# Optimization experiments

Measured on AMD Instinct MI355X. Metric: run time of the kernel, lower is better.

The kernel has to match this reference:

```python
import jax, jax.numpy as jnp
import numpy as np

N = 204800   # total nodes (4096 subgraphs x 50 nodes)
E = 3276800  # edges (avg degree 16)
B = 4096     # number of subgraphs
IN = 64      # in_feats
HID = 32     # latent_dim per layer
CAT = 128    # 4 * 32 concatenated states
PH = 64      # pooling hidden dim
R = 3        # num_relations
NB = 2       # num_bases
MARGIN = 1.0


def setup_inputs() -> dict:
    key = jax.random.key(0)
    ks = jax.random.split(key, 24)
    s = 0.1
    inp = {}
    inp['x'] = jax.random.normal(ks[0], (N, IN), jnp.float32)
    inp['edge_norm'] = jax.random.uniform(ks[1], (E,), jnp.float32)
    inp['src'] = jax.random.randint(ks[2], (E,), 0, N, jnp.int32)
    inp['dst'] = jax.random.randint(ks[3], (E,), 0, N, jnp.int32)
    inp['etype'] = jax.random.randint(ks[4], (E,), 0, R, jnp.int32)
    inp['graph_id'] = jnp.arange(N, dtype=jnp.int32) // (N // B)
    inp['ntype'] = jax.random.randint(ks[5], (N,), 0, 2, jnp.int32)
    # layer 0: basis-decomposed RelGraphConv (in=64 -> 32)
    inp['bases0'] = jax.random.normal(ks[6], (NB, IN, HID), jnp.float32) * s
    inp['coef0'] = jax.random.normal(ks[7], (R, NB), jnp.float32)
    inp['wself0'] = jax.random.normal(ks[8], (IN, HID), jnp.float32) * s
    inp['bias0'] = jnp.zeros((HID,), jnp.float32)
    # layers 1..3 stacked (32 -> 32 each)
    inp['bases_r'] = jax.random.normal(ks[9], (3, NB, HID, HID), jnp.float32) * s
    inp['coef_r'] = jax.random.normal(ks[10], (3, R, NB), jnp.float32)
    inp['wself_r'] = jax.random.normal(ks[11], (3, HID, HID), jnp.float32) * s
    inp['bias_r'] = jnp.zeros((3, HID), jnp.float32)
    # attention pooling (user / item)
    inp['wp_u'] = jax.random.normal(ks[12], (CAT, PH), jnp.float32) * s
    inp['wt_u'] = jax.random.normal(ks[13], (CAT, PH), jnp.float32) * s
    inp['wp_i'] = jax.random.normal(ks[14], (CAT, PH), jnp.float32) * s
    inp['wt_i'] = jax.random.normal(ks[15], (CAT, PH), jnp.float32) * s
    # MLP head
    inp['w1'] = jax.random.normal(ks[16], (2 * PH, 64), jnp.float32) * s
    inp['b1'] = jnp.zeros((64,), jnp.float32)
    inp['w2'] = jax.random.normal(ks[17], (64, 1), jnp.float32) * s
    inp['b2'] = jnp.zeros((1,), jnp.float32)
    return inp


def _rgcn_layer(h, bases, coef, wself, bias, src, dst, etype, edge_norm):
    # basis decomposition: W_r = sum_b coef[r,b] * bases[b]
    W = jnp.einsum('rb,bio->rio', coef, bases)          # [R, in, out]
    xr = jnp.einsum('ni,rio->nro', h, W)                # [N, R, out] (transform then gather)
    msg = xr[src, etype] * edge_norm[:, None]           # [E, out]
    agg = jax.ops.segment_sum(msg, dst, num_segments=N) # scatter-add to dst
    return jnp.tanh(agg + h @ wself + bias)


def _attn_pool(x, mask, gid, wp, wt):
    # x: [N, CAT], mask: [N] bool (target node type), gid: [N] graph ids
    fmask = mask.astype(x.dtype)
    cnt = jax.ops.segment_sum(fmask, gid, num_segments=B)              # [B]
    tmean = jax.ops.segment_sum(x * fmask[:, None], gid, num_segments=B)
    tmean = tmean / (cnt[:, None] + 1e-8)                              # [B, CAT]
    p = x @ wp                                                          # [N, PH]
    t = tmean @ wt                                                      # [B, PH]
    score = jnp.sum(p * t[gid], axis=-1) / jnp.sqrt(jnp.float32(PH))    # [N]
    score = jnp.where(mask, score, -1e9)
    m = jax.ops.segment_max(score, gid, num_segments=B)                 # [B]
    a = jnp.exp(score - m[gid]) * fmask
    z = jax.ops.segment_sum(a, gid, num_segments=B)
    alpha = a / (z[gid] + 1e-8)
    return jax.ops.segment_sum(alpha[:, None] * p, gid, num_segments=B)  # [B, PH]


def reference(x, edge_norm, src, dst, etype, graph_id, ntype,
              bases0, coef0, wself0, bias0, bases_r, coef_r, wself_r, bias_r,
              wp_u, wt_u, wp_i, wt_i, w1, b1, w2, b2):
    h = x
    states = []
    h = _rgcn_layer(h, bases0, coef0, wself0, bias0, src, dst, etype, edge_norm)
    states.append(h)
    for l in range(3):
        h = _rgcn_layer(h, bases_r[l], coef_r[l], wself_r[l], bias_r[l],
                        src, dst, etype, edge_norm)
        states.append(h)
    hcat = jnp.concatenate(states, axis=1)  # [N, 128]

    mask_u = ntype == 0
    mask_i = ntype == 1

    # triplet contrastive loss over per-graph mean user/item embeddings
    fu = mask_u.astype(hcat.dtype)
    fi = mask_i.astype(hcat.dtype)
    cu = jax.ops.segment_sum(fu, graph_id, num_segments=B) + 1e-8
    ci = jax.ops.segment_sum(fi, graph_id, num_segments=B) + 1e-8
    au = jax.ops.segment_sum(hcat * fu[:, None], graph_id, num_segments=B) / cu[:, None]
    ai = jax.ops.segment_sum(hcat * fi[:, None], graph_id, num_segments=B) / ci[:, None]
    an = jnp.roll(ai, 1, axis=0)  # negatives from shifted graphs
    dpos = jnp.sum((au - ai) ** 2, axis=-1)
    dneg = jnp.sum((au - an) ** 2, axis=-1)
    triplet_loss = jnp.mean(jax.nn.relu(dpos - dneg + MARGIN))

    x_u = _attn_pool(hcat, mask_u, graph_id, wp_u, wt_u)  # [B, 64]
    x_i = _attn_pool(hcat, mask_i, graph_id, wp_i, wt_i)  # [B, 64]
    z = jnp.concatenate([x_u, x_i], axis=1)               # [B, 128]
    z = jax.nn.relu(z @ w1 + b1)                          # dropout off (eval)
    out = jax.nn.sigmoid(z @ w2 + b2)[:, 0]               # [B]
    return out, triplet_loss
```

## Files before the change

### kernel.cpp

```cpp
#include <hip/hip_runtime.h>
#include <cstdint>
#include <cstddef>

#define NN   204800
#define EE   3276800
#define BB   4096
#define GS   50
#define NBUCK 200
#define CHUNK 8192
#define BCAP  17408

typedef __attribute__((ext_vector_type(8))) short short8v;
typedef __attribute__((ext_vector_type(4))) float f32x4;

__device__ __forceinline__ float bf2f(unsigned short u) {
  unsigned int x = ((unsigned int)u) << 16;
  return __int_as_float((int)x);
}
__device__ __forceinline__ unsigned short f2bf(float f) {
  unsigned int x = __float_as_uint(f);
  unsigned int r = (x + 0x7fffu + ((x >> 16) & 1u)) >> 16;
  return (unsigned short)r;
}

__global__ __launch_bounds__(256) void init_cursor_kernel(int* __restrict__ gcursor) {
  const int t = threadIdx.x;
  if (t < NBUCK) gcursor[t] = t * BCAP;
}

__global__ __launch_bounds__(256) void pass1_kernel(const int* __restrict__ src,
                                                    const int* __restrict__ dst,
                                                    const int* __restrict__ etype,
                                                    const float* __restrict__ en,
                                                    int* __restrict__ gcursor,
                                                    int2* __restrict__ staging) {
  __shared__ int2 stage[CHUNK];
  __shared__ unsigned char bid[CHUNK];
  __shared__ int hist[NBUCK], cur[NBUCK], lo[NBUCK], gbase[NBUCK];
  __shared__ int sc[256];
  const int tid = threadIdx.x;
  const int ebase = blockIdx.x * CHUNK;

  for (int i = tid; i < NBUCK; i += 256) hist[i] = 0;
  __syncthreads();
  for (int i = tid; i < CHUNK; i += 256) {
    int bk = dst[ebase + i] >> 10;
    bid[i] = (unsigned char)bk;
    atomicAdd(&hist[bk], 1);
  }
  __syncthreads();
  int hv = (tid < NBUCK) ? hist[tid] : 0;
  sc[tid] = hv;
  __syncthreads();
  for (int off = 1; off < 256; off <<= 1) {
    int t = (tid >= off) ? sc[tid - off] : 0;
    __syncthreads();
    sc[tid] += t;
    __syncthreads();
  }
  if (tid < NBUCK) {
    int excl = sc[tid] - hv;
    lo[tid]  = excl;
    cur[tid] = excl;
    gbase[tid] = hv ? atomicAdd(&gcursor[tid], hv) : 0;
  }
  __syncthreads();
  for (int i = tid; i < CHUNK; i += 256) {
    int bk = bid[i];
    int p = atomicAdd(&cur[bk], 1);
    int s  = src[ebase + i];
    int et = etype[ebase + i];
    int d  = dst[ebase + i];
    int2 r;
    r.x = (s << 12) | (et << 10) | (d & 1023);
    r.y = __float_as_int(en[ebase + i]);
    stage[p] = r;
  }
  __syncthreads();
  const int wave = tid >> 6, lane = tid & 63;
  for (int bk = wave; bk < NBUCK; bk += 4) {
    const int len = hist[bk];
    const int l0  = lo[bk];
    const int gb  = gbase[bk];
    for (int i = lane; i < len; i += 64)
      staging[gb + i] = stage[l0 + i];
  }
}

__global__ __launch_bounds__(256) void pass2_kernel(const int2* __restrict__ staging,
                                                    const int* __restrict__ gcursor,
                                                    int* __restrict__ begs,
                                                    int* __restrict__ ends,
                                                    int2* __restrict__ edata) {
  __shared__ int lhist[1024];
  __shared__ int lcur[1024];
  __shared__ int psum[256];
  const int b = blockIdx.x;
  const int tid = threadIdx.x;
  const int base = b * BCAP;
  const int cnt  = gcursor[b] - base;

  for (int i = tid; i < 1024; i += 256) lhist[i] = 0;
  __syncthreads();
  for (int i = tid; i < cnt; i += 256)
    atomicAdd(&lhist[staging[base + i].x & 1023], 1);
  __syncthreads();
  int s0 = lhist[4 * tid], s1 = lhist[4 * tid + 1];
  int s2 = lhist[4 * tid + 2], s3 = lhist[4 * tid + 3];
  int tot = s0 + s1 + s2 + s3;
  psum[tid] = tot;
  __syncthreads();
  for (int off = 1; off < 256; off <<= 1) {
    int t = (tid >= off) ? psum[tid - off] : 0;
    __syncthreads();
    psum[tid] += t;
    __syncthreads();
  }
  int o0 = base + psum[tid] - tot;
  int o1 = o0 + s0, o2 = o1 + s1, o3 = o2 + s2;
  const int nodeb = b * 1024;
  begs[nodeb + 4 * tid]     = o0;  ends[nodeb + 4 * tid]     = o1;  lcur[4 * tid]     = o0;
  begs[nodeb + 4 * tid + 1] = o1;  ends[nodeb + 4 * tid + 1] = o2;  lcur[4 * tid + 1] = o1;
  begs[nodeb + 4 * tid + 2] = o2;  ends[nodeb + 4 * tid + 2] = o3;  lcur[4 * tid + 2] = o2;
  begs[nodeb + 4 * tid + 3] = o3;  ends[nodeb + 4 * tid + 3] = o3 + s3;  lcur[4 * tid + 3] = o3;
  __syncthreads();
  for (int i = tid; i < cnt; i += 256) {
    int2 r = staging[base + i];
    int pos = atomicAdd(&lcur[r.x & 1023], 1);
    int s  = r.x >> 12;
    int et = (r.x >> 10) & 3;
    int2 outr;
    outr.x = (s << 8) + (et << 6);
    outr.y = r.y;
    edata[pos] = outr;
  }
}

__global__ __launch_bounds__(256) void wprep_kernel(
    const float* __restrict__ bases0, const float* __restrict__ coef0,
    const float* __restrict__ wself0,
    const float* __restrict__ bases_r, const float* __restrict__ coef_r,
    const float* __restrict__ wself_r,
    const float* __restrict__ wp_u, const float* __restrict__ wp_i,
    const float* __restrict__ wt_u, const float* __restrict__ wt_i,
    const float* __restrict__ w1,
    float* __restrict__ Wbuf) {
  int idx = blockIdx.x * 256 + threadIdx.x;
  if (idx < 8192) {
    int i = idx >> 7, j = idx & 127;
    float v;
    if (j < 96) {
      int r = j >> 5, f = j & 31;
      v = coef0[r * 2 + 0] * bases0[0 * 2048 + i * 32 + f]
        + coef0[r * 2 + 1] * bases0[1 * 2048 + i * 32 + f];
    } else {
      v = wself0[i * 32 + (j - 96)];
    }
    Wbuf[idx] = v;
    return;
  }
  int idx2 = idx - 8192;
  if (idx2 < 3 * 4096) {
    int l = idx2 >> 12, rem = idx2 & 4095;
    int i = rem >> 7, j = rem & 127;
    float v;
    if (j < 96) {
      int r = j >> 5, f = j & 31;
      v = coef_r[l * 6 + r * 2 + 0] * bases_r[l * 2048 + 0 * 1024 + i * 32 + f]
        + coef_r[l * 6 + r * 2 + 1] * bases_r[l * 2048 + 1 * 1024 + i * 32 + f];
    } else {
      v = wself_r[l * 1024 + i * 32 + (j - 96)];
    }
    Wbuf[idx] = v;
    return;
  }
  int idx3 = idx2 - 12288;
  if (idx3 < 32768) {
    int side = idx3 >> 14;
    int r = idx3 & 16383;
    int kk = r >> 7, k = r & 127;
    const float* wp = side ? wp_i : wp_u;
    const float* wt = side ? wt_i : wt_u;
    float acc = 0.f;
#pragma unroll 8
    for (int j = 0; j < 64; ++j)
      acc = fmaf(wp[k * 64 + j], wt[kk * 64 + j], acc);
    Wbuf[idx] = acc * 0.125f;
    return;
  }
  int idx4 = idx3 - 32768;
  if (idx4 < 16384) {
    int kp = idx4 >> 6, t = idx4 & 63;
    int side = kp >> 7, k = kp & 127;
    const float* wp = side ? wp_i : wp_u;
    float acc = 0.f;
#pragma unroll 8
    for (int j = 0; j < 64; ++j)
      acc = fmaf(wp[k * 64 + j], w1[(side * 64 + j) * 64 + t], acc);
    Wbuf[idx] = acc;
  }
}

__global__ __launch_bounds__(256) void wprep2_kernel(const float* __restrict__ Wbuf,
                                                     unsigned short* __restrict__ Whi,
                                                     unsigned short* __restrict__ Wlo) {
  int e = blockIdx.x * 256 + threadIdx.x;
  if (e >= 20480) return;
  float v;
  if (e < 8192) {
    int j = e & 7, l = (e >> 3) & 63, c = (e >> 9) & 7, q = e >> 12;
    int k   = q * 32 + (l >> 4) * 8 + j;
    int col = c * 16 + (l & 15);
    v = Wbuf[k * 128 + col];
  } else {
    int e2 = e - 8192;
    int lay = e2 >> 12, r = e2 & 4095;
    int j = r & 7, l = (r >> 3) & 63, qc = r >> 9;
    int q = qc >> 1, c = qc & 1;
    int k = q * 32 + (l >> 4) * 8 + j;
    int o = c * 16 + (l & 15);
    const float* Wc = Wbuf + 8192 + lay * 4096;
    v = (k < 96) ? Wc[(k & 31) * 128 + (k >> 5) * 32 + o]
                 : Wc[(k - 96) * 128 + 96 + o];
  }
  unsigned short hi = f2bf(v);
  Whi[e] = hi;
  Wlo[e] = f2bf(v - bf2f(hi));
}

__global__ __launch_bounds__(256) void cvt_bf16_kernel(const float* __restrict__ in,
                                                       unsigned short* __restrict__ hi,
                                                       unsigned short* __restrict__ lo,
                                                       int n4) {
  int i = blockIdx.x * 256 + threadIdx.x;
  if (i < n4) {
    const float4 a = reinterpret_cast<const float4*>(in)[i];
    ushort4 h, l;
    h.x = f2bf(a.x); l.x = f2bf(a.x - bf2f(h.x));
    h.y = f2bf(a.y); l.y = f2bf(a.y - bf2f(h.y));
    h.z = f2bf(a.z); l.z = f2bf(a.z - bf2f(h.z));
    h.w = f2bf(a.w); l.w = f2bf(a.w - bf2f(h.w));
    reinterpret_cast<ushort4*>(hi)[i] = h;
    reinterpret_cast<ushort4*>(lo)[i] = l;
  }
}

__global__ __launch_bounds__(256) void transform_l0_kernel(
    const unsigned short* __restrict__ Ahi, const unsigned short* __restrict__ Alo,
    const unsigned short* __restrict__ Whi, const unsigned short* __restrict__ Wlo,
    unsigned short* __restrict__ Tb0) {
  __shared__ float C[64][129];
  const int tid = threadIdx.x;
  const int wv = tid >> 6, l = tid & 63;
  const int l15 = l & 15, kg = l >> 4;
  const int row = blockIdx.x * 64 + wv * 16 + l15;

  short8v ah[2], al[2];
#pragma unroll
  for (int q = 0; q < 2; ++q) {
    ah[q] = *reinterpret_cast<const short8v*>(Ahi + (size_t)row * 64 + q * 32 + kg * 8);
    al[q] = *reinterpret_cast<const short8v*>(Alo + (size_t)row * 64 + q * 32 + kg * 8);
  }

#pragma unroll
  for (int c = 0; c < 8; ++c) {
    f32x4 a = {0.f, 0.f, 0.f, 0.f};
#pragma unroll
    for (int q = 0; q < 2; ++q) {
      const size_t fb = ((size_t)(q * 8 + c) * 64 + l) * 8;
      const short8v bh = *reinterpret_cast<const short8v*>(Whi + fb);
      const short8v bl = *reinterpret_cast<const short8v*>(Wlo + fb);
      a = __builtin_amdgcn_mfma_f32_16x16x32_bf16(ah[q], bh, a, 0, 0, 0);
      a = __builtin_amdgcn_mfma_f32_16x16x32_bf16(al[q], bh, a, 0, 0, 0);
      a = __builtin_amdgcn_mfma_f32_16x16x32_bf16(ah[q], bl, a, 0, 0, 0);
    }
#pragma unroll
    for (int r = 0; r < 4; ++r)
      C[wv * 16 + kg * 4 + r][c * 16 + l15] = a[r];
  }
  __syncthreads();

  const int row64 = tid & 63, q = tid >> 6;
  const int node = blockIdx.x * 64 + row64;
#pragma unroll
  for (int v = 0; v < 4; ++v) {
    const int cb = q * 32 + v * 8;
    uint4 pk;
    pk.x = (unsigned)f2bf(C[row64][cb + 0]) | ((unsigned)f2bf(C[row64][cb + 1]) << 16);
    pk.y = (unsigned)f2bf(C[row64][cb + 2]) | ((unsigned)f2bf(C[row64][cb + 3]) << 16);
    pk.z = (unsigned)f2bf(C[row64][cb + 4]) | ((unsigned)f2bf(C[row64][cb + 5]) << 16);
    pk.w = (unsigned)f2bf(C[row64][cb + 6]) | ((unsigned)f2bf(C[row64][cb + 7]) << 16);
    *reinterpret_cast<uint4*>(Tb0 + (size_t)node * 128 + cb) = pk;
  }
}

__global__ __launch_bounds__(256) void aggregate_l0_kernel(
    const unsigned short* __restrict__ Tb0,
    const int* __restrict__ begs, const int* __restrict__ ends,
    const int2* __restrict__ edata, const float* __restrict__ bias,
    float* __restrict__ hcat, unsigned short* __restrict__ Ab) {
  const int node = blockIdx.x * 32 + (threadIdx.x >> 3);
  const int f4   = (threadIdx.x & 7) * 4;
  const int loff = f4 * 2;
  const char* Tbc = (const char*)Tb0;
  const int beg = begs[node];
  const int end = ends[node];
  const ushort4 sb = *reinterpret_cast<const ushort4*>(Tbc + (size_t)node * 256 + 192 + loff);
  const float4 bv  = *reinterpret_cast<const float4*>(&bias[f4]);
  float ax = bf2f(sb.x) + bv.x, ay = bf2f(sb.y) + bv.y;
  float az = bf2f(sb.z) + bv.z, aw = bf2f(sb.w) + bv.w;

  int k = beg;
  for (; k + 8 <= end; k += 8) {
    int2 ed[8];
#pragma unroll
    for (int u = 0; u < 8; ++u) ed[u] = edata[k + u];
    ushort4 mv[8];
#pragma unroll
    for (int u = 0; u < 8; ++u)
      mv[u] = *reinterpret_cast<const ushort4*>(Tbc + ed[u].x + loff);
#pragma unroll
    for (int u = 0; u < 8; ++u) {
      const float nm = __int_as_float(ed[u].y);
      ax = fmaf(bf2f(mv[u].x), nm, ax);
      ay = fmaf(bf2f(mv[u].y), nm, ay);
      az = fmaf(bf2f(mv[u].z), nm, az);
      aw = fmaf(bf2f(mv[u].w), nm, aw);
    }
  }
  for (; k < end; ++k) {
    int2 e0 = edata[k];
    const float nm = __int_as_float(e0.y);
    ushort4 m0 = *reinterpret_cast<const ushort4*>(Tbc + e0.x + loff);
    ax = fmaf(bf2f(m0.x), nm, ax);
    ay = fmaf(bf2f(m0.y), nm, ay);
    az = fmaf(bf2f(m0.z), nm, az);
    aw = fmaf(bf2f(m0.w), nm, aw);
  }
  float4 o;
  o.x = tanhf(ax); o.y = tanhf(ay); o.z = tanhf(az); o.w = tanhf(aw);
  *reinterpret_cast<float4*>(&hcat[(size_t)node * 128 + f4]) = o;
  ushort4 h;
  h.x = f2bf(o.x); h.y = f2bf(o.y); h.z = f2bf(o.z); h.w = f2bf(o.w);
  *reinterpret_cast<ushort4*>(Ab + (size_t)node * 128 + 96 + f4) = h;
}

__global__ __launch_bounds__(256) void aggregate_raw_kernel(
    unsigned short* __restrict__ Ab,
    const int* __restrict__ begs, const int* __restrict__ ends,
    const int2* __restrict__ edata) {
  const int node = blockIdx.x * 32 + (threadIdx.x >> 3);
  const int f4   = (threadIdx.x & 7) * 4;
  const int loff = f4 * 2;
  const char* Abc = (const char*)Ab;
  const int beg = begs[node];
  const int end = ends[node];
  float a0x = 0.f, a0y = 0.f, a0z = 0.f, a0w = 0.f;
  float a1x = 0.f, a1y = 0.f, a1z = 0.f, a1w = 0.f;
  float a2x = 0.f, a2y = 0.f, a2z = 0.f, a2w = 0.f;

  int k = beg;
  for (; k + 8 <= end; k += 8) {
    int2 ed[8];
#pragma unroll
    for (int u = 0; u < 8; ++u) ed[u] = edata[k + u];
    ushort4 mv[8];
#pragma unroll
    for (int u = 0; u < 8; ++u)
      mv[u] = *reinterpret_cast<const ushort4*>(Abc + (ed[u].x & ~255) + 192 + loff);
#pragma unroll
    for (int u = 0; u < 8; ++u) {
      const int et = (ed[u].x >> 6) & 3;
      const float nm = __int_as_float(ed[u].y);
      const float n0 = (et == 0) ? nm : 0.f;
      const float n1 = (et == 1) ? nm : 0.f;
      const float n2 = (et == 2) ? nm : 0.f;
      const float vx = bf2f(mv[u].x), vy = bf2f(mv[u].y);
      const float vz = bf2f(mv[u].z), vw = bf2f(mv[u].w);
      a0x = fmaf(vx, n0, a0x); a0y = fmaf(vy, n0, a0y);
      a0z = fmaf(vz, n0, a0z); a0w = fmaf(vw, n0, a0w);
      a1x = fmaf(vx, n1, a1x); a1y = fmaf(vy, n1, a1y);
      a1z = fmaf(vz, n1, a1z); a1w = fmaf(vw, n1, a1w);
      a2x = fmaf(vx, n2, a2x); a2y = fmaf(vy, n2, a2y);
      a2z = fmaf(vz, n2, a2z); a2w = fmaf(vw, n2, a2w);
    }
  }
  for (; k < end; ++k) {
    int2 e0 = edata[k];
    const int et = (e0.x >> 6) & 3;
    const float nm = __int_as_float(e0.y);
    const float n0 = (et == 0) ? nm : 0.f;
    const float n1 = (et == 1) ? nm : 0.f;
    const float n2 = (et == 2) ? nm : 0.f;
    ushort4 m0 = *reinterpret_cast<const ushort4*>(Abc + (e0.x & ~255) + 192 + loff);
    const float vx = bf2f(m0.x), vy = bf2f(m0.y), vz = bf2f(m0.z), vw = bf2f(m0.w);
    a0x = fmaf(vx, n0, a0x); a0y = fmaf(vy, n0, a0y);
    a0z = fmaf(vz, n0, a0z); a0w = fmaf(vw, n0, a0w);
    a1x = fmaf(vx, n1, a1x); a1y = fmaf(vy, n1, a1y);
    a1z = fmaf(vz, n1, a1z); a1w = fmaf(vw, n1, a1w);
    a2x = fmaf(vx, n2, a2x); a2y = fmaf(vy, n2, a2y);
    a2z = fmaf(vz, n2, a2z); a2w = fmaf(vw, n2, a2w);
  }
  ushort4 s0, s1, s2;
  s0.x = f2bf(a0x); s0.y = f2bf(a0y); s0.z = f2bf(a0z); s0.w = f2bf(a0w);
  s1.x = f2bf(a1x); s1.y = f2bf(a1y); s1.z = f2bf(a1z); s1.w = f2bf(a1w);
  s2.x = f2bf(a2x); s2.y = f2bf(a2y); s2.z = f2bf(a2z); s2.w = f2bf(a2w);
  unsigned short* rowp = Ab + (size_t)node * 128;
  *reinterpret_cast<ushort4*>(rowp + f4)      = s0;
  *reinterpret_cast<ushort4*>(rowp + 32 + f4) = s1;
  *reinterpret_cast<ushort4*>(rowp + 64 + f4) = s2;
}

__global__ __launch_bounds__(256) void transform_new_kernel(
    const unsigned short* __restrict__ Ab,
    const unsigned short* __restrict__ Whi, const unsigned short* __restrict__ Wlo,
    const float* __restrict__ bias,
    float* __restrict__ hcatSlot, unsigned short* __restrict__ AbY) {
  __shared__ float C[64][33];
  const int tid = threadIdx.x;
  const int wv = tid >> 6, l = tid & 63;
  const int l15 = l & 15, kg = l >> 4;
  const int row = blockIdx.x * 64 + wv * 16 + l15;

  short8v af[4];
#pragma unroll
  for (int q = 0; q < 4; ++q)
    af[q] = *reinterpret_cast<const short8v*>(Ab + (size_t)row * 128 + q * 32 + kg * 8);

#pragma unroll
  for (int c = 0; c < 2; ++c) {
    f32x4 a = {0.f, 0.f, 0.f, 0.f};
#pragma unroll
    for (int q = 0; q < 4; ++q) {
      const size_t fb = ((size_t)(q * 2 + c) * 64 + l) * 8;
      const short8v bh = *reinterpret_cast<const short8v*>(Whi + fb);
      const short8v bl = *reinterpret_cast<const short8v*>(Wlo + fb);
      a = __builtin_amdgcn_mfma_f32_16x16x32_bf16(af[q], bh, a, 0, 0, 0);
      a = __builtin_amdgcn_mfma_f32_16x16x32_bf16(af[q], bl, a, 0, 0, 0);
    }
#pragma unroll
    for (int r = 0; r < 4; ++r)
      C[wv * 16 + kg * 4 + r][c * 16 + l15] = a[r];
  }
  __syncthreads();

  const int row64 = tid & 63, g = tid >> 6;
  const int node = blockIdx.x * 64 + row64;
  float z[8];
#pragma unroll
  for (int v = 0; v < 8; ++v)
    z[v] = tanhf(C[row64][g * 8 + v] + bias[g * 8 + v]);
  float4 f0 = {z[0], z[1], z[2], z[3]};
  float4 f1 = {z[4], z[5], z[6], z[7]};
  *reinterpret_cast<float4*>(hcatSlot + (size_t)node * 128 + g * 8)     = f0;
  *reinterpret_cast<float4*>(hcatSlot + (size_t)node * 128 + g * 8 + 4) = f1;
  if (AbY) {
    uint4 pk;
    pk.x = (unsigned)f2bf(z[0]) | ((unsigned)f2bf(z[1]) << 16);
    pk.y = (unsigned)f2bf(z[2]) | ((unsigned)f2bf(z[3]) << 16);
    pk.z = (unsigned)f2bf(z[4]) | ((unsigned)f2bf(z[5]) << 16);
    pk.w = (unsigned)f2bf(z[6]) | ((unsigned)f2bf(z[7]) << 16);
    *reinterpret_cast<uint4*>(AbY + (size_t)node * 128 + 96 + g * 8) = pk;
  }
}

__global__ __launch_bounds__(256) void pool_head_kernel(
    const float* __restrict__ hcat, const int* __restrict__ ntype,
    const float* __restrict__ Mt,
    const float* __restrict__ W1c,
    const float* __restrict__ b1,
    const float* __restrict__ w2, const float* __restrict__ b2,
    float* __restrict__ out, float* __restrict__ tl) {
  __shared__ float hl[GS * 129];
  __shared__ float scr[1024];
  __shared__ float av2[256];
  __shared__ float red[4];
  __shared__ float cnts[4];
  __shared__ int   snt[64];
  __shared__ int   sntp[64];

  const int g    = (blockIdx.x & 7) * (BB / 8) + (blockIdx.x >> 3);
  const int gp   = (g + BB - 1) & (BB - 1);
  const int tid  = threadIdx.x;
  const int lane = tid & 63;

  const float* hg  = hcat + (size_t)g  * (GS * 128);
  const float* hp  = hcat + (size_t)gp * (GS * 128);
  const int*   ntg = ntype + g  * GS;
  const int*   ntp = ntype + gp * GS;

  if (tid < 64) {
    snt[tid] = (tid < GS) ? ntg[tid] : 99;
    unsigned long long bu = __ballot(snt[tid] == 0);
    unsigned long long bi = __ballot(snt[tid] == 1);
    if (lane == 0) {
      cnts[0] = 1.f / ((float)__popcll(bu) + 1e-8f);
      cnts[1] = 1.f / ((float)__popcll(bi) + 1e-8f);
    }
  } else if (tid < 128) {
    sntp[lane] = (lane < GS) ? ntp[lane] : 99;
    unsigned long long bp = __ballot(sntp[lane] == 1);
    if (lane == 0) cnts[2] = 1.f / ((float)__popcll(bp) + 1e-8f);
  }

  {
    const int rowg = tid >> 5;
    const int kq   = (tid & 31) * 4;
    float spx = 0.f, spy = 0.f, spz = 0.f, spw = 0.f;
#pragma unroll
    for (int p = 0; p < 7; ++p) {
      const int r = rowg + 8 * p;
      if (r < GS) {
        const float4 v = *reinterpret_cast<const float4*>(hg + r * 128 + kq);
        hl[r * 129 + kq + 0] = v.x;
        hl[r * 129 + kq + 1] = v.y;
        hl[r * 129 + kq + 2] = v.z;
        hl[r * 129 + kq + 3] = v.w;
        if (ntp[r] == 1) {
          const float4 w = *reinterpret_cast<const float4*>(hp + r * 128 + kq);
          spx += w.x; spy += w.y; spz += w.z; spw += w.w;
        }
      }
    }
    scr[rowg * 128 + kq + 0] = spx;
    scr[rowg * 128 + kq + 1] = spy;
    scr[rowg * 128 + kq + 2] = spz;
    scr[rowg * 128 + kq + 3] = spw;
  }
  __syncthreads();

  if (tid < 128) {
    const int kf = tid;
    float su = 0.f, si = 0.f;
#pragma unroll
    for (int r = 0; r < GS; ++r) {
      const float v = hl[r * 129 + kf];
      if (snt[r] == 0) su += v; else si += v;
    }
    float sp = 0.f;
#pragma unroll
    for (int rg = 0; rg < 8; ++rg) sp += scr[rg * 128 + kf];
    const float auk = su * cnts[0];
    const float aik = si * cnts[1];
    const float apk = sp * cnts[2];
    av2[kf]       = auk;
    av2[128 + kf] = aik;
    float d1 = (auk - aik) * (auk - aik);
    float d2 = (auk - apk) * (auk - apk);
    for (int o = 32; o; o >>= 1) {
      d1 += __shfl_xor(d1, o);
      d2 += __shfl_xor(d2, o);
    }
    if (lane == 0) { red[tid >> 6] = d1; red[2 + (tid >> 6)] = d2; }
  }
  __syncthreads();

  {
    const int side = tid >> 7, kf = tid & 127;
    const float* M  = Mt + (size_t)side * 16384 + kf;
    const float* av = av2 + side * 128;
    float a0 = 0.f, a1 = 0.f, a2 = 0.f, a3 = 0.f;
#pragma unroll 4
    for (int kk = 0; kk < 128; kk += 4) {
      a0 = fmaf(M[(kk + 0) * 128], av[kk + 0], a0);
      a1 = fmaf(M[(kk + 1) * 128], av[kk + 1], a1);
      a2 = fmaf(M[(kk + 2) * 128], av[kk + 2], a2);
      a3 = fmaf(M[(kk + 3) * 128], av[kk + 3], a3);
    }
    scr[tid] = (a0 + a1) + (a2 + a3);
  }
  if (tid == 0) tl[g] = fmaxf(0.f, (red[0] + red[1]) - (red[2] + red[3]) + 1.0f);
  __syncthreads();

  if (tid < 128) {
    const int side = tid >> 6;
    const float* q = scr + side * 128;
    float v = -1e9f;
    bool msk = false;
    if (lane < GS) {
      msk = (snt[lane] == side);
      float a0 = 0.f, a1 = 0.f;
#pragma unroll 8
      for (int k = 0; k < 128; k += 2) {
        a0 = fmaf(hl[lane * 129 + k], q[k], a0);
        a1 = fmaf(hl[lane * 129 + k + 1], q[k + 1], a1);
      }
      v = msk ? (a0 + a1) : -1e9f;
    }
    float m = v;
    for (int o = 32; o; o >>= 1) m = fmaxf(m, __shfl_xor(m, o));
    float e = (lane < GS && msk) ? expf(v - m) : 0.f;
    float z = e;
    for (int o = 32; o; o >>= 1) z += __shfl_xor(z, o);
    const float invz = 1.f / (z + 1e-8f);
    if (lane < GS) scr[256 + side * 64 + lane] = e * invz;
  }
  __syncthreads();

  {
    const int side = tid >> 7, kf = tid & 127;
    const float* a = scr + 256 + side * 64;
    float acc = 0.f;
#pragma unroll
    for (int nl = 0; nl < GS; ++nl)
      acc = fmaf(a[nl], hl[nl * 129 + kf], acc);
    scr[384 + side * 128 + kf] = acc;
  }
  __syncthreads();

  {
    const int j = tid & 63, c = tid >> 6;
    const float* Wc = W1c + (size_t)c * 64 * 64 + j;
    const float* cv = scr + 384 + c * 64;
    float a0 = 0.f, a1 = 0.f, a2 = 0.f, a3 = 0.f;
#pragma unroll 4
    for (int k = 0; k < 64; k += 4) {
      a0 = fmaf(Wc[(k + 0) * 64], cv[k + 0], a0);
      a1 = fmaf(Wc[(k + 1) * 64], cv[k + 1], a1);
      a2 = fmaf(Wc[(k + 2) * 64], cv[k + 2], a2);
      a3 = fmaf(Wc[(k + 3) * 64], cv[k + 3], a3);
    }
    scr[640 + c * 64 + j] = (a0 + a1) + (a2 + a3);
  }
  __syncthreads();

  if (tid < 64) {
    const float z1 = fmaxf(b1[tid] + scr[640 + tid] + scr[704 + tid] +
                           scr[768 + tid] + scr[832 + tid], 0.f);
    float p = z1 * w2[tid];
    for (int o = 32; o; o >>= 1) p += __shfl_xor(p, o);
    if (tid == 0) out[g] = 1.f / (1.f + expf(-(p + b2[0])));
  }
}

__global__ __launch_bounds__(256) void tl_reduce_kernel(const float* __restrict__ tl,
                                                        float* __restrict__ out) {
  __shared__ float s[256];
  float acc = 0.f;
  for (int i = threadIdx.x; i < BB; i += 256) acc += tl[i];
  s[threadIdx.x] = acc;
  __syncthreads();
  for (int off = 128; off > 0; off >>= 1) {
    if (threadIdx.x < off) s[threadIdx.x] += s[threadIdx.x + off];
    __syncthreads();
  }
  if (threadIdx.x == 0) out[BB] = s[0] * (1.f / (float)BB);
}

extern "C" void kernel_launch(void* const* d_in, const int* in_sizes, int n_in,
                              void* d_out, int out_size, void* d_ws, size_t ws_size,
                              hipStream_t stream) {
  const float* x        = (const float*)d_in[0];
  const float* edge_nrm = (const float*)d_in[1];
  const int*   src      = (const int*)d_in[2];
  const int*   dst      = (const int*)d_in[3];
  const int*   etype    = (const int*)d_in[4];
  const int*   ntype    = (const int*)d_in[6];
  const float* bases0   = (const float*)d_in[7];
  const float* coef0    = (const float*)d_in[8];
  const float* wself0   = (const float*)d_in[9];
  const float* bias0    = (const float*)d_in[10];
  const float* bases_r  = (const float*)d_in[11];
  const float* coef_r   = (const float*)d_in[12];
  const float* wself_r  = (const float*)d_in[13];
  const float* bias_r   = (const float*)d_in[14];
  const float* wp_u     = (const float*)d_in[15];
  const float* wt_u     = (const float*)d_in[16];
  const float* wp_i     = (const float*)d_in[17];
  const float* wt_i     = (const float*)d_in[18];
  const float* w1       = (const float*)d_in[19];
  const float* b1       = (const float*)d_in[20];
  const float* w2       = (const float*)d_in[21];
  const float* b2       = (const float*)d_in[22];
  float* out = (float*)d_out;

  float*          hcat = (float*)d_ws;
  float*          R    = hcat + (size_t)NN * 128;
  int2*           staging = (int2*)R;
  unsigned short* Tb0  = (unsigned short*)R;
  unsigned short* AbA  = Tb0 + (size_t)NN * 128;
  unsigned short* AbB  = Tb0;
  unsigned short* A0hi = (unsigned short*)(hcat + (size_t)NN * 64);
  unsigned short* A0lo = A0hi + (size_t)NN * 64;
  int2*  edata   = (int2*)(R + (size_t)NN * 128);
  int*   begs    = (int*)(edata + (size_t)NBUCK * BCAP);
  int*   ends    = begs + NN;
  int*   gcursor = ends + NN;
  float* Wbuf    = (float*)(gcursor + 256);
  unsigned short* Whi = (unsigned short*)(Wbuf + 69632);
  unsigned short* Wlo = Whi + 20480;
  float* tl      = Wbuf + 69632 + 10240;

  size_t need = ((size_t)NN * 128 * 2 + (size_t)NBUCK * BCAP * 2 + 2 * NN + 256 +
                 69632 + 10240 + BB) * 4;
  if (ws_size < need) return;

  init_cursor_kernel<<<1, 256, 0, stream>>>(gcursor);
  pass1_kernel<<<EE / CHUNK, 256, 0, stream>>>(src, dst, etype, edge_nrm,
                                               gcursor, staging);
  pass2_kernel<<<NBUCK, 256, 0, stream>>>(staging, gcursor, begs, ends, edata);

  wprep_kernel<<<(69632 + 255) / 256, 256, 0, stream>>>(
      bases0, coef0, wself0, bases_r, coef_r, wself_r,
      wp_u, wp_i, wt_u, wt_i, w1, Wbuf);
  wprep2_kernel<<<80, 256, 0, stream>>>(Wbuf, Whi, Wlo);
  cvt_bf16_kernel<<<(NN * 64 / 4 + 255) / 256, 256, 0, stream>>>(
      x, A0hi, A0lo, NN * 64 / 4);

  transform_l0_kernel<<<NN / 64, 256, 0, stream>>>(A0hi, A0lo, Whi, Wlo, Tb0);
  aggregate_l0_kernel<<<NN / 32, 256, 0, stream>>>(Tb0, begs, ends, edata,
                                                   bias0, hcat, AbA);

  unsigned short* AbX[3] = {AbA, AbB, AbA};
  unsigned short* AbY[3] = {AbB, AbA, nullptr};
  for (int l = 1; l <= 3; ++l) {
    aggregate_raw_kernel<<<NN / 32, 256, 0, stream>>>(AbX[l - 1], begs, ends, edata);
    transform_new_kernel<<<NN / 64, 256, 0, stream>>>(
        AbX[l - 1], Whi + 8192 + (size_t)(l - 1) * 4096,
        Wlo + 8192 + (size_t)(l - 1) * 4096, bias_r + (l - 1) * 32,
        hcat + (size_t)l * 32, AbY[l - 1]);
  }

  pool_head_kernel<<<BB, 256, 0, stream>>>(hcat, ntype,
                                           Wbuf + 20480, Wbuf + 53248,
                                           b1, w2, b2, out, tl);
  tl_reduce_kernel<<<1, 256, 0, stream>>>(tl, out);
}
```

Before: 589.2 us.

## Fuse edge aggregation with per-layer transform and fold bf16 split into L0 transform

```diff
diff --git a/kernel.cpp b/kernel.cpp
--- a/kernel.cpp
+++ b/kernel.cpp
@@ -21,11 +21,6 @@
   unsigned int x = __float_as_uint(f);
   unsigned int r = (x + 0x7fffu + ((x >> 16) & 1u)) >> 16;
   return (unsigned short)r;
-}
-
-__global__ __launch_bounds__(256) void init_cursor_kernel(int* __restrict__ gcursor) {
-  const int t = threadIdx.x;
-  if (t < NBUCK) gcursor[t] = t * BCAP;
 }
 
 __global__ __launch_bounds__(256) void pass1_kernel(const int* __restrict__ src,
@@ -144,7 +139,9 @@
     const float* __restrict__ wp_u, const float* __restrict__ wp_i,
     const float* __restrict__ wt_u, const float* __restrict__ wt_i,
     const float* __restrict__ w1,
-    float* __restrict__ Wbuf) {
+    float* __restrict__ Wbuf, int* __restrict__ gcursor) {
+  if (blockIdx.x == 0 && threadIdx.x < NBUCK)
+    gcursor[threadIdx.x] = threadIdx.x * BCAP;
   int idx = blockIdx.x * 256 + threadIdx.x;
   if (idx < 8192) {
     int i = idx >> 7, j = idx & 127;
@@ -228,25 +225,8 @@
   Wlo[e] = f2bf(v - bf2f(hi));
 }
 
-__global__ __launch_bounds__(256) void cvt_bf16_kernel(const float* __restrict__ in,
-                                                       unsigned short* __restrict__ hi,
-                                                       unsigned short* __restrict__ lo,
-                                                       int n4) {
-  int i = blockIdx.x * 256 + threadIdx.x;
-  if (i < n4) {
-    const float4 a = reinterpret_cast<const float4*>(in)[i];
-    ushort4 h, l;
-    h.x = f2bf(a.x); l.x = f2bf(a.x - bf2f(h.x));
-    h.y = f2bf(a.y); l.y = f2bf(a.y - bf2f(h.y));
-    h.z = f2bf(a.z); l.z = f2bf(a.z - bf2f(h.z));
-    h.w = f2bf(a.w); l.w = f2bf(a.w - bf2f(h.w));
-    reinterpret_cast<ushort4*>(hi)[i] = h;
-    reinterpret_cast<ushort4*>(lo)[i] = l;
-  }
-}
-
 __global__ __launch_bounds__(256) void transform_l0_kernel(
-    const unsigned short* __restrict__ Ahi, const unsigned short* __restrict__ Alo,
+    const float* __restrict__ x,
     const unsigned short* __restrict__ Whi, const unsigned short* __restrict__ Wlo,
     unsigned short* __restrict__ Tb0) {
   __shared__ float C[64][129];
@@ -258,8 +238,16 @@
   short8v ah[2], al[2];
 #pragma unroll
   for (int q = 0; q < 2; ++q) {
-    ah[q] = *reinterpret_cast<const short8v*>(Ahi + (size_t)row * 64 + q * 32 + kg * 8);
-    al[q] = *reinterpret_cast<const short8v*>(Alo + (size_t)row * 64 + q * 32 + kg * 8);
+    const float* xp = x + (size_t)row * 64 + q * 32 + kg * 8;
+    const float4 v0 = *reinterpret_cast<const float4*>(xp);
+    const float4 v1 = *reinterpret_cast<const float4*>(xp + 4);
+    const float vv[8] = {v0.x, v0.y, v0.z, v0.w, v1.x, v1.y, v1.z, v1.w};
+#pragma unroll
+    for (int f = 0; f < 8; ++f) {
+      const unsigned short h = f2bf(vv[f]);
+      ah[q][f] = (short)h;
+      al[q][f] = (short)f2bf(vv[f] - bf2f(h));
+    }
   }
 
 #pragma unroll
@@ -298,7 +286,7 @@
     const unsigned short* __restrict__ Tb0,
     const int* __restrict__ begs, const int* __restrict__ ends,
     const int2* __restrict__ edata, const float* __restrict__ bias,
-    float* __restrict__ hcat, unsigned short* __restrict__ Ab) {
+    float* __restrict__ hcat, unsigned short* __restrict__ hbA) {
   const int node = blockIdx.x * 32 + (threadIdx.x >> 3);
   const int f4   = (threadIdx.x & 7) * 4;
   const int loff = f4 * 2;
@@ -342,125 +330,128 @@
   *reinterpret_cast<float4*>(&hcat[(size_t)node * 128 + f4]) = o;
   ushort4 h;
   h.x = f2bf(o.x); h.y = f2bf(o.y); h.z = f2bf(o.z); h.w = f2bf(o.w);
-  *reinterpret_cast<ushort4*>(Ab + (size_t)node * 128 + 96 + f4) = h;
-}
-
-__global__ __launch_bounds__(256) void aggregate_raw_kernel(
-    unsigned short* __restrict__ Ab,
+  *reinterpret_cast<ushort4*>(hbA + (size_t)node * 32 + f4) = h;
+}
+
+__global__ __launch_bounds__(256) void agg_tf_kernel(
+    const unsigned short* __restrict__ hbX,
     const int* __restrict__ begs, const int* __restrict__ ends,
-    const int2* __restrict__ edata) {
-  const int node = blockIdx.x * 32 + (threadIdx.x >> 3);
-  const int f4   = (threadIdx.x & 7) * 4;
-  const int loff = f4 * 2;
-  const char* Abc = (const char*)Ab;
-  const int beg = begs[node];
-  const int end = ends[node];
-  float a0x = 0.f, a0y = 0.f, a0z = 0.f, a0w = 0.f;
-  float a1x = 0.f, a1y = 0.f, a1z = 0.f, a1w = 0.f;
-  float a2x = 0.f, a2y = 0.f, a2z = 0.f, a2w = 0.f;
-
-  int k = beg;
-  for (; k + 8 <= end; k += 8) {
-    int2 ed[8];
-#pragma unroll
-    for (int u = 0; u < 8; ++u) ed[u] = edata[k + u];
-    ushort4 mv[8];
-#pragma unroll
-    for (int u = 0; u < 8; ++u)
-      mv[u] = *reinterpret_cast<const ushort4*>(Abc + (ed[u].x & ~255) + 192 + loff);
-#pragma unroll
-    for (int u = 0; u < 8; ++u) {
-      const int et = (ed[u].x >> 6) & 3;
-      const float nm = __int_as_float(ed[u].y);
+    const int2* __restrict__ edata,
+    const unsigned short* __restrict__ Whi, const unsigned short* __restrict__ Wlo,
+    const float* __restrict__ bias,
+    float* __restrict__ hcatSlot, unsigned short* __restrict__ hbY) {
+  __shared__ __align__(16) unsigned short sld[64][136];
+  __shared__ float C[64][33];
+  const int tid = threadIdx.x;
+
+  {
+    const int nl   = tid >> 2;
+    const int node = blockIdx.x * 64 + nl;
+    const int f8   = (tid & 3) * 8;
+    const int loff = f8 * 2;
+    const char* hbc = (const char*)hbX;
+    const int beg = begs[node], end = ends[node];
+    float a0[8], a1[8], a2[8];
+#pragma unroll
+    for (int f = 0; f < 8; ++f) { a0[f] = 0.f; a1[f] = 0.f; a2[f] = 0.f; }
+
+    int k = beg;
+    for (; k + 8 <= end; k += 8) {
+      int2 ed[8];
+#pragma unroll
+      for (int u = 0; u < 8; ++u) ed[u] = edata[k + u];
+      short8v mv[8];
+#pragma unroll
+      for (int u = 0; u < 8; ++u)
+        mv[u] = *reinterpret_cast<const short8v*>(hbc + ((ed[u].x >> 2) & ~63) + loff);
+#pragma unroll
+      for (int u = 0; u < 8; ++u) {
+        const int et = (ed[u].x >> 6) & 3;
+        const float nm = __int_as_float(ed[u].y);
+        const float n0 = (et == 0) ? nm : 0.f;
+        const float n1 = (et == 1) ? nm : 0.f;
+        const float n2 = (et == 2) ? nm : 0.f;
+#pragma unroll
+        for (int f = 0; f < 8; ++f) {
+          const float v = bf2f((unsigned short)mv[u][f]);
+          a0[f] = fmaf(v, n0, a0[f]);
+          a1[f] = fmaf(v, n1, a1[f]);
+          a2[f] = fmaf(v, n2, a2[f]);
+        }
+      }
+    }
+    for (; k < end; ++k) {
+      int2 e0 = edata[k];
+      const int et = (e0.x >> 6) & 3;
+      const float nm = __int_as_float(e0.y);
       const float n0 = (et == 0) ? nm : 0.f;
       const float n1 = (et == 1) ? nm : 0.f;
       const float n2 = (et == 2) ? nm : 0.f;
-      const float vx = bf2f(mv[u].x), vy = bf2f(mv[u].y);
-      const float vz = bf2f(mv[u].z), vw = bf2f(mv[u].w);
-      a0x = fmaf(vx, n0, a0x); a0y = fmaf(vy, n0, a0y);
-      a0z = fmaf(vz, n0, a0z); a0w = fmaf(vw, n0, a0w);
-      a1x = fmaf(vx, n1, a1x); a1y = fmaf(vy, n1, a1y);
-      a1z = fmaf(vz, n1, a1z); a1w = fmaf(vw, n1, a1w);
-      a2x = fmaf(vx, n2, a2x); a2y = fmaf(vy, n2, a2y);
-      a2z = fmaf(vz, n2, a2z); a2w = fmaf(vw, n2, a2w);
-    }
-  }
-  for (; k < end; ++k) {
-    int2 e0 = edata[k];
-    const int et = (e0.x >> 6) & 3;
-    const float nm = __int_as_float(e0.y);
-    const float n0 = (et == 0) ? nm : 0.f;
-    const float n1 = (et == 1) ? nm : 0.f;
-    const float n2 = (et == 2) ? nm : 0.f;
-    ushort4 m0 = *reinterpret_cast<const ushort4*>(Abc + (e0.x & ~255) + 192 + loff);
-    const float vx = bf2f(m0.x), vy = bf2f(m0.y), vz = bf2f(m0.z), vw = bf2f(m0.w);
-    a0x = fmaf(vx, n0, a0x); a0y = fmaf(vy, n0, a0y);
-    a0z = fmaf(vz, n0, a0z); a0w = fmaf(vw, n0, a0w);
-    a1x = fmaf(vx, n1, a1x); a1y = fmaf(vy, n1, a1y);
-    a1z = fmaf(vz, n1, a1z); a1w = fmaf(vw, n1, a1w);
-    a2x = fmaf(vx, n2, a2x); a2y = fmaf(vy, n2, a2y);
-    a2z = fmaf(vz, n2, a2z); a2w = fmaf(vw, n2, a2w);
-  }
-  ushort4 s0, s1, s2;
-  s0.x = f2bf(a0x); s0.y = f2bf(a0y); s0.z = f2bf(a0z); s0.w = f2bf(a0w);
-  s1.x = f2bf(a1x); s1.y = f2bf(a1y); s1.z = f2bf(a1z); s1.w = f2bf(a1w);
-  s2.x = f2bf(a2x); s2.y = f2bf(a2y); s2.z = f2bf(a2z); s2.w = f2bf(a2w);
-  unsigned short* rowp = Ab + (size_t)node * 128;
-  *reinterpret_cast<ushort4*>(rowp + f4)      = s0;
-  *reinterpret_cast<ushort4*>(rowp + 32 + f4) = s1;
-  *reinterpret_cast<ushort4*>(rowp + 64 + f4) = s2;
-}
-
-__global__ __launch_bounds__(256) void transform_new_kernel(
-    const unsigned short* __restrict__ Ab,
-    const unsigned short* __restrict__ Whi, const unsigned short* __restrict__ Wlo,
-    const float* __restrict__ bias,
-    float* __restrict__ hcatSlot, unsigned short* __restrict__ AbY) {
-  __shared__ float C[64][33];
-  const int tid = threadIdx.x;
-  const int wv = tid >> 6, l = tid & 63;
-  const int l15 = l & 15, kg = l >> 4;
-  const int row = blockIdx.x * 64 + wv * 16 + l15;
-
-  short8v af[4];
-#pragma unroll
-  for (int q = 0; q < 4; ++q)
-    af[q] = *reinterpret_cast<const short8v*>(Ab + (size_t)row * 128 + q * 32 + kg * 8);
-
-#pragma unroll
-  for (int c = 0; c < 2; ++c) {
-    f32x4 a = {0.f, 0.f, 0.f, 0.f};
-#pragma unroll
-    for (int q = 0; q < 4; ++q) {
-      const size_t fb = ((size_t)(q * 2 + c) * 64 + l) * 8;
-      const short8v bh = *reinterpret_cast<const short8v*>(Whi + fb);
-      const short8v bl = *reinterpret_cast<const short8v*>(Wlo + fb);
-      a = __builtin_amdgcn_mfma_f32_16x16x32_bf16(af[q], bh, a, 0, 0, 0);
-      a = __builtin_amdgcn_mfma_f32_16x16x32_bf16(af[q], bl, a, 0, 0, 0);
-    }
-#pragma unroll
-    for (int r = 0; r < 4; ++r)
-      C[wv * 16 + kg * 4 + r][c * 16 + l15] = a[r];
-  }
-  __syncthreads();
-
-  const int row64 = tid & 63, g = tid >> 6;
-  const int node = blockIdx.x * 64 + row64;
-  float z[8];
-#pragma unroll
-  for (int v = 0; v < 8; ++v)
-    z[v] = tanhf(C[row64][g * 8 + v] + bias[g * 8 + v]);
-  float4 f0 = {z[0], z[1], z[2], z[3]};
-  float4 f1 = {z[4], z[5], z[6], z[7]};
-  *reinterpret_cast<float4*>(hcatSlot + (size_t)node * 128 + g * 8)     = f0;
-  *reinterpret_cast<float4*>(hcatSlot + (size_t)node * 128 + g * 8 + 4) = f1;
-  if (AbY) {
-    uint4 pk;
-    pk.x = (unsigned)f2bf(z[0]) | ((unsigned)f2bf(z[1]) << 16);
-    pk.y = (unsigned)f2bf(z[2]) | ((unsigned)f2bf(z[3]) << 16);
-    pk.z = (unsigned)f2bf(z[4]) | ((unsigned)f2bf(z[5]) << 16);
-    pk.w = (unsigned)f2bf(z[6]) | ((unsigned)f2bf(z[7]) << 16);
-    *reinterpret_cast<uint4*>(AbY + (size_t)node * 128 + 96 + g * 8) = pk;
+      const short8v m0 = *reinterpret_cast<const short8v*>(hbc + ((e0.x >> 2) & ~63) + loff);
+#pragma unroll
+      for (int f = 0; f < 8; ++f) {
+        const float v = bf2f((unsigned short)m0[f]);
+        a0[f] = fmaf(v, n0, a0[f]);
+        a1[f] = fmaf(v, n1, a1[f]);
+        a2[f] = fmaf(v, n2, a2[f]);
+      }
+    }
+#pragma unroll
+    for (int f = 0; f < 8; ++f) {
+      sld[nl][f8 + f]      = f2bf(a0[f]);
+      sld[nl][32 + f8 + f] = f2bf(a1[f]);
+      sld[nl][64 + f8 + f] = f2bf(a2[f]);
+    }
+    *reinterpret_cast<short8v*>(&sld[nl][96 + f8]) =
+        *reinterpret_cast<const short8v*>(hbX + (size_t)node * 32 + f8);
+  }
+  __syncthreads();
+
+  {
+    const int wv = tid >> 6, l = tid & 63;
+    const int l15 = l & 15, kg = l >> 4;
+    const int row = wv * 16 + l15;
+    short8v af[4];
+#pragma unroll
+    for (int q = 0; q < 4; ++q)
+      af[q] = *reinterpret_cast<const short8v*>(&sld[row][q * 32 + kg * 8]);
+#pragma unroll
+    for (int c = 0; c < 2; ++c) {
+      f32x4 a = {0.f, 0.f, 0.f, 0.f};
+#pragma unroll
+      for (int q = 0; q < 4; ++q) {
+        const size_t fb = ((size_t)(q * 2 + c) * 64 + l) * 8;
+        const short8v bh = *reinterpret_cast<const short8v*>(Whi + fb);
+        const short8v bl = *reinterpret_cast<const short8v*>(Wlo + fb);
+        a = __builtin_amdgcn_mfma_f32_16x16x32_bf16(af[q], bh, a, 0, 0, 0);
+        a = __builtin_amdgcn_mfma_f32_16x16x32_bf16(af[q], bl, a, 0, 0, 0);
+      }
+#pragma unroll
+      for (int r = 0; r < 4; ++r)
+        C[wv * 16 + kg * 4 + r][c * 16 + l15] = a[r];
+    }
+  }
+  __syncthreads();
+
+  {
+    const int row64 = tid & 63, g = tid >> 6;
+    const int node = blockIdx.x * 64 + row64;
+    float z[8];
+#pragma unroll
+    for (int v = 0; v < 8; ++v)
+      z[v] = tanhf(C[row64][g * 8 + v] + bias[g * 8 + v]);
+    float4 f0 = {z[0], z[1], z[2], z[3]};
+    float4 f1 = {z[4], z[5], z[6], z[7]};
+    *reinterpret_cast<float4*>(hcatSlot + (size_t)node * 128 + g * 8)     = f0;
+    *reinterpret_cast<float4*>(hcatSlot + (size_t)node * 128 + g * 8 + 4) = f1;
+    if (hbY) {
+      uint4 pk;
+      pk.x = (unsigned)f2bf(z[0]) | ((unsigned)f2bf(z[1]) << 16);
+      pk.y = (unsigned)f2bf(z[2]) | ((unsigned)f2bf(z[3]) << 16);
+      pk.z = (unsigned)f2bf(z[4]) | ((unsigned)f2bf(z[5]) << 16);
+      pk.w = (unsigned)f2bf(z[6]) | ((unsigned)f2bf(z[7]) << 16);
+      *reinterpret_cast<uint4*>(hbY + (size_t)node * 32 + g * 8) = pk;
+    }
   }
 }
 
@@ -678,10 +669,8 @@
   float*          R    = hcat + (size_t)NN * 128;
   int2*           staging = (int2*)R;
   unsigned short* Tb0  = (unsigned short*)R;
-  unsigned short* AbA  = Tb0 + (size_t)NN * 128;
-  unsigned short* AbB  = Tb0;
-  unsigned short* A0hi = (unsigned short*)(hcat + (size_t)NN * 64);
-  unsigned short* A0lo = A0hi + (size_t)NN * 64;
+  unsigned short* hbA  = Tb0 + (size_t)NN * 128;
+  unsigned short* hbB  = hbA + (size_t)NN * 32;
   int2*  edata   = (int2*)(R + (size_t)NN * 128);
   int*   begs    = (int*)(edata + (size_t)NBUCK * BCAP);
   int*   ends    = begs + NN;
@@ -695,31 +684,28 @@
                  69632 + 10240 + BB) * 4;
   if (ws_size < need) return;
 
-  init_cursor_kernel<<<1, 256, 0, stream>>>(gcursor);
+  wprep_kernel<<<(69632 + 255) / 256, 256, 0, stream>>>(
+      bases0, coef0, wself0, bases_r, coef_r, wself_r,
+      wp_u, wp_i, wt_u, wt_i, w1, Wbuf, gcursor);
+  wprep2_kernel<<<80, 256, 0, stream>>>(Wbuf, Whi, Wlo);
+
   pass1_kernel<<<EE / CHUNK, 256, 0, stream>>>(src, dst, etype, edge_nrm,
                                                gcursor, staging);
   pass2_kernel<<<NBUCK, 256, 0, stream>>>(staging, gcursor, begs, ends, edata);
 
-  wprep_kernel<<<(69632 + 255) / 256, 256, 0, stream>>>(
-      bases0, coef0, wself0, bases_r, coef_r, wself_r,
-      wp_u, wp_i, wt_u, wt_i, w1, Wbuf);
-  wprep2_kernel<<<80, 256, 0, stream>>>(Wbuf, Whi, Wlo);
-  cvt_bf16_kernel<<<(NN * 64 / 4 + 255) / 256, 256, 0, stream>>>(
-      x, A0hi, A0lo, NN * 64 / 4);
-
-  transform_l0_kernel<<<NN / 64, 256, 0, stream>>>(A0hi, A0lo, Whi, Wlo, Tb0);
+  transform_l0_kernel<<<NN / 64, 256, 0, stream>>>(x, Whi, Wlo, Tb0);
   aggregate_l0_kernel<<<NN / 32, 256, 0, stream>>>(Tb0, begs, ends, edata,
-                                                   bias0, hcat, AbA);
-
-  unsigned short* AbX[3] = {AbA, AbB, AbA};
-  unsigned short* AbY[3] = {AbB, AbA, nullptr};
-  for (int l = 1; l <= 3; ++l) {
-    aggregate_raw_kernel<<<NN / 32, 256, 0, stream>>>(AbX[l - 1], begs, ends, edata);
-    transform_new_kernel<<<NN / 64, 256, 0, stream>>>(
-        AbX[l - 1], Whi + 8192 + (size_t)(l - 1) * 4096,
-        Wlo + 8192 + (size_t)(l - 1) * 4096, bias_r + (l - 1) * 32,
-        hcat + (size_t)l * 32, AbY[l - 1]);
-  }
+                                                   bias0, hcat, hbA);
+
+  agg_tf_kernel<<<NN / 64, 256, 0, stream>>>(
+      hbA, begs, ends, edata, Whi + 8192, Wlo + 8192, bias_r,
+      hcat + 32, hbB);
+  agg_tf_kernel<<<NN / 64, 256, 0, stream>>>(
+      hbB, begs, ends, edata, Whi + 12288, Wlo + 12288, bias_r + 32,
+      hcat + 64, hbA);
+  agg_tf_kernel<<<NN / 64, 256, 0, stream>>>(
+      hbA, begs, ends, edata, Whi + 16384, Wlo + 16384, bias_r + 64,
+      hcat + 96, nullptr);
 
   pool_head_kernel<<<BB, 256, 0, stream>>>(hcat, ntype,
                                            Wbuf + 20480, Wbuf + 53248,
```

Result: faster. 550.6 us (-6.6%).
